# Kernel optimization log

Hardware: AMD Instinct MI355X
Metric: run time of the kernel (lower is better)

The kernel has to match this reference:

```python
import jax, jax.numpy as jnp
import numpy as np

# --- model dims (from init args) ---
LAYERS = 6
LEAF = 2 ** (LAYERS - 1)        # 32
M_LEN = 128
CAM_NUM = 2
MAIN_CAM = 0
LATENT = 48
H_LAT = 2048                    # LatentNet hidden
H_BR = 512                      # ChooseBranchNet hidden
B = 16384

# Path bits: for leaf i, bit at classifier depth d (root->leaf order) is
# (i >> (LAYERS-2-d)) & 1. This is exactly what the search_table + double
# advanced-indexing gather in the torch code computes (heap tree routing).
_BITS = ((np.arange(LEAF)[:, None] >> np.arange(LAYERS - 2, -1, -1)[None, :]) & 1)  # [LEAF, LAYERS-1]
BITS = jnp.asarray(_BITS, dtype=jnp.int32)


def setup_inputs() -> dict:
    key = jax.random.key(0)
    ks = jax.random.split(key, 9)
    s = lambda fan: 1.0 / np.sqrt(fan)
    return {
        "batch_data": jax.random.normal(ks[0], (B, CAM_NUM, M_LEN), dtype=jnp.float32),
        # LatentNet: [B, 2*M_LEN] -> hidden -> LEAF*LATENT
        "Wl1": jax.random.normal(ks[1], (2 * M_LEN, H_LAT), dtype=jnp.float32) * s(2 * M_LEN),
        "bl1": jnp.zeros((H_LAT,), dtype=jnp.float32),
        "Wl2": jax.random.normal(ks[2], (H_LAT, LEAF * LATENT), dtype=jnp.float32) * s(H_LAT),
        "bl2": jnp.zeros((LEAF * LATENT,), dtype=jnp.float32),
        # ChooseBranchNet (shared across the LAYERS-1 classifier slots): M_LEN -> hidden -> 2
        "Wb1": jax.random.normal(ks[3], (M_LEN, H_BR), dtype=jnp.float32) * s(M_LEN),
        "bb1": jnp.zeros((H_BR,), dtype=jnp.float32),
        "Wb2": jax.random.normal(ks[4], (H_BR, 2), dtype=jnp.float32) * s(H_BR),
        "bb2": jnp.zeros((2,), dtype=jnp.float32),
    }


def reference(batch_data, Wl1, bl1, Wl2, bl2, Wb1, bb1, Wb2, bb2):
    bsz = batch_data.shape[0]
    # expand_measurements: main cam repeated (LAYERS-1) times -> [B, LAYERS-1, M_LEN]
    main = batch_data[:, MAIN_CAM]                                  # [B, M_LEN]
    x_br = jnp.broadcast_to(main[:, None, :], (bsz, LAYERS - 1, M_LEN))
    # ChooseBranchNet -> per-layer 2-way probabilities
    h = jax.nn.relu(jnp.einsum('blm,mh->blh', x_br, Wb1) + bb1)
    p = jax.nn.softmax(jnp.einsum('blh,ho->blo', h, Wb2) + bb2, axis=-1)  # [B, L-1, 2]
    # Tree gates: product of path-branch probabilities along root->leaf path.
    comp = jnp.where(BITS[None] == 1, p[:, None, :, 1], p[:, None, :, 0])  # [B, LEAF, L-1]
    gates = jnp.prod(comp, axis=-1)                                        # [B, LEAF]
    # top-1 routing (argsort(...)[:, -1] as in the torch code)
    router = jnp.argsort(gates, axis=-1)[:, -1]                            # [B]
    # LatentNet on concatenated two-camera measurements
    x2 = jnp.concatenate([batch_data[:, 0], batch_data[:, 1]], axis=-1)    # [B, 2*M_LEN]
    hl = jax.nn.relu(x2 @ Wl1 + bl1)
    nn_latent = (hl @ Wl2 + bl2).reshape(bsz, LEAF, LATENT)
    # scatter-select per-sample leaf latent (replaces the torch.where loop)
    select = jnp.take_along_axis(nn_latent, router[:, None, None], axis=1)[:, 0]  # [B, LATENT]
    return select
```

## Files before the change

kernel.cpp:

```cpp
#include <hip/hip_runtime.h>
#include <stdint.h>

typedef short bf16x8 __attribute__((ext_vector_type(8)));
typedef float f32x4 __attribute__((ext_vector_type(4)));

#define NROWS 16384
#define K1DIM 256
#define N1DIM 2048
#define N2DIM 96
#define MARGIN 0.03f

#define GLD16(g, l) __builtin_amdgcn_global_load_lds( \
    (const __attribute__((address_space(1))) uint32_t*)(g), \
    (__attribute__((address_space(3))) uint32_t*)(l), 16, 0, 0)

__device__ __forceinline__ ushort f2bf(float x) {
  union { float f; uint32_t u; } c; c.f = x;
  uint32_t u = c.u;
  return (ushort)((u + 0x7FFFu + ((u >> 16) & 1u)) >> 16);
}

__global__ __launch_bounds__(256) void k0_convert(
    const float* __restrict__ bd, const float* __restrict__ Wl1,
    const float* __restrict__ Wl2, const float* __restrict__ Wb1,
    ushort* __restrict__ x2bf, ushort* __restrict__ wl1t,
    ushort* __restrict__ w2t, ushort* __restrict__ wb1t) {
  int i = blockIdx.x * 256 + threadIdx.x;
  if (i < NROWS * 256) x2bf[i] = f2bf(bd[i]);
  if (i < 2048 * 256) {
    int n = i >> 8, k = i & 255;
    wl1t[i] = f2bf(Wl1[k * 2048 + n]);
  }
  if (i < 96 * 2048) {
    int j = i >> 11, k = i & 2047;
    int col = (j < 48) ? j : (1440 + j);
    w2t[i] = f2bf(Wl2[k * 1536 + col]);
  }
  if (i < 512 * 128) {
    int j = i >> 7, m = i & 127;
    wb1t[i] = f2bf(Wb1[m * 512 + j]);
  }
}

__global__ __launch_bounds__(256) void k1a_score(
    const ushort* __restrict__ x2bf, const ushort* __restrict__ wb1t,
    const float* __restrict__ bb1, const float* __restrict__ Wb2,
    float* __restrict__ part) {
  __shared__ __align__(1024) ushort As[128 * 64];
  __shared__ __align__(1024) ushort Bs[128 * 64];
  const int t = threadIdx.x, ln = t & 63, wv = t >> 6;
  const int m0 = blockIdx.y << 7;
  const int n0 = blockIdx.x << 7;
  const int wm = (wv >> 1) << 6, wn = (wv & 1) << 6;
  const int rsub = ln >> 3, kc8 = ln & 7;
  const int q = ln >> 4, rr = ln & 15;

  f32x4 acc[4][4] = {};

  for (int k0 = 0; k0 < 128; k0 += 64) {
#pragma unroll
    for (int i = 0; i < 4; i++) {
      int inst = (wv << 2) + i;
      int row = (inst << 3) + rsub;
      GLD16(x2bf + (size_t)(m0 + row) * 256 + k0 + (kc8 << 3), As + (inst << 9));
      GLD16(wb1t + (size_t)(n0 + row) * 128 + k0 + (kc8 << 3), Bs + (inst << 9));
    }
    __syncthreads();
#pragma unroll
    for (int kk = 0; kk < 2; kk++) {
      int kb = ((kk << 2) + q) << 3;
      bf16x8 af[4], bfr[4];
#pragma unroll
      for (int mi = 0; mi < 4; mi++)
        af[mi] = *(const bf16x8*)(As + (((wm + (mi << 4) + rr)) << 6) + kb);
#pragma unroll
      for (int ni = 0; ni < 4; ni++)
        bfr[ni] = *(const bf16x8*)(Bs + (((wn + (ni << 4) + rr)) << 6) + kb);
#pragma unroll
      for (int mi = 0; mi < 4; mi++)
#pragma unroll
        for (int ni = 0; ni < 4; ni++)
          acc[mi][ni] = __builtin_amdgcn_mfma_f32_16x16x32_bf16(
              af[mi], bfr[ni], acc[mi][ni], 0, 0, 0);
    }
    __syncthreads();
  }

  float s4[4][4] = {};
#pragma unroll
  for (int ni = 0; ni < 4; ni++) {
    int col = n0 + wn + (ni << 4) + rr;
    float bias = bb1[col];
    float wdv = Wb2[col * 2 + 1] - Wb2[col * 2];
#pragma unroll
    for (int mi = 0; mi < 4; mi++) {
      f32x4 a = acc[mi][ni];
#pragma unroll
      for (int v = 0; v < 4; v++)
        s4[mi][v] += fmaxf(a[v] + bias, 0.f) * wdv;
    }
  }
#pragma unroll
  for (int off = 1; off <= 8; off <<= 1)
#pragma unroll
    for (int mi = 0; mi < 4; mi++)
#pragma unroll
      for (int v = 0; v < 4; v++)
        s4[mi][v] += __shfl_xor(s4[mi][v], off);

  if (rr == 0) {
    float* dst = part + (size_t)(blockIdx.x * 2 + (wv & 1)) * NROWS +
                 m0 + wm + (q << 2);
#pragma unroll
    for (int mi = 0; mi < 4; mi++) {
      float4 v4 = make_float4(s4[mi][0], s4[mi][1], s4[mi][2], s4[mi][3]);
      *(float4*)(dst + (mi << 4)) = v4;
    }
  }
}

__global__ __launch_bounds__(256) void k1b_classify(
    const float* __restrict__ part, const float* __restrict__ bb2,
    int* __restrict__ router, int* __restrict__ list, int* __restrict__ counter) {
  int t = blockIdx.x * 256 + threadIdx.x;
  float s = bb2[1] - bb2[0];
#pragma unroll
  for (int i = 0; i < 8; i++) s += part[i * NROWS + t];
  router[t] = (s >= 0.f) ? 1 : 0;
  if (fabsf(s) < MARGIN) {
    int idx = atomicAdd(counter, 1);
    list[idx] = t;
  }
}

__global__ __launch_bounds__(256) void k1c_recheck(
    const float* __restrict__ bd, const float* __restrict__ Wb1,
    const float* __restrict__ Wb2, const float* __restrict__ bb1,
    const float* __restrict__ bb2, const int* __restrict__ list,
    const int* __restrict__ counter, int* __restrict__ router) {
  const int ln = threadIdx.x & 63;
  const int wid = (blockIdx.x * 256 + threadIdx.x) >> 6;
  const int count = *counter;
  const float c = bb2[1] - bb2[0];

  for (int base = wid * 4; base < count; base += 512 * 4) {
    int rows[4];
#pragma unroll
    for (int r = 0; r < 4; r++) {
      int idx = base + r;
      rows[r] = list[(idx < count) ? idx : base];
    }
    float acc[4][8];
#pragma unroll
    for (int r = 0; r < 4; r++)
#pragma unroll
      for (int u = 0; u < 8; u++) acc[r][u] = 0.f;

    for (int m = 0; m < 128; m++) {
      float w[8];
#pragma unroll
      for (int u = 0; u < 8; u++) w[u] = Wb1[m * 512 + (u << 6) + ln];
#pragma unroll
      for (int r = 0; r < 4; r++) {
        float x = bd[(size_t)rows[r] * 256 + m];
#pragma unroll
        for (int u = 0; u < 8; u++) acc[r][u] = fmaf(x, w[u], acc[r][u]);
      }
    }
    float sc[4];
#pragma unroll
    for (int r = 0; r < 4; r++) {
      float s = 0.f;
#pragma unroll
      for (int u = 0; u < 8; u++) {
        int j = (u << 6) + ln;
        float wd = Wb2[j * 2 + 1] - Wb2[j * 2];
        s += fmaxf(acc[r][u] + bb1[j], 0.f) * wd;
      }
#pragma unroll
      for (int off = 1; off <= 32; off <<= 1) s += __shfl_xor(s, off);
      sc[r] = s + c;
    }
    if (ln == 0) {
#pragma unroll
      for (int r = 0; r < 4; r++)
        if (base + r < count) router[rows[r]] = (sc[r] >= 0.f) ? 1 : 0;
    }
  }
}

__global__ __launch_bounds__(256) void k2_fused(
    const ushort* __restrict__ x2bf, const ushort* __restrict__ wl1t,
    const ushort* __restrict__ w2t, const float* __restrict__ bl1,
    const float* __restrict__ bl2, const int* __restrict__ router,
    float* __restrict__ out) {
  __shared__ __align__(1024) ushort As[64 * 64];
  __shared__ __align__(1024) ushort Bs[128 * 64];
  __shared__ __align__(1024) ushort Ws[2 * 96 * 64];
  __shared__ __align__(1024) ushort Hs[64 * 128];
  const int t = threadIdx.x, ln = t & 63, wv = t >> 6;
  const int ks2 = blockIdx.x;
  const int m0 = blockIdx.y << 6;
  const int q = ln >> 4, rr = ln & 15;
  const int rsub = ln >> 3;
  const int swz8 = ((ln & 7) ^ rsub) << 3;

  f32x4 accP[6] = {};

  for (int nc = 0; nc < 8; nc++) {
    const int n0 = (ks2 << 10) + (nc << 7);

#pragma unroll
    for (int j = 0; j < 6; j++) {
      int inst = wv * 6 + j;
      int h = inst / 12;
      int r12 = inst - h * 12;
      GLD16(w2t + (size_t)((r12 << 3) + rsub) * 2048 + n0 + (h << 6) + swz8,
            Ws + h * 6144 + (r12 << 9));
    }

    f32x4 acc1[4][2] = {};
    for (int k0 = 0; k0 < K1DIM; k0 += 64) {
#pragma unroll
      for (int i = 0; i < 2; i++) {
        int inst = (wv << 1) + i;
        GLD16(x2bf + (size_t)(m0 + (inst << 3) + rsub) * K1DIM + k0 + swz8,
              As + (inst << 9));
      }
#pragma unroll
      for (int i = 0; i < 4; i++) {
        int inst = (wv << 2) + i;
        GLD16(wl1t + (size_t)(n0 + (inst << 3) + rsub) * K1DIM + k0 + swz8,
              Bs + (inst << 9));
      }
      __syncthreads();
#pragma unroll
      for (int kk = 0; kk < 2; kk++) {
        int slot = ((kk << 2) + q);
        bf16x8 af[4], bfr[2];
#pragma unroll
        for (int mi = 0; mi < 4; mi++)
          af[mi] = *(const bf16x8*)(As + (((mi << 4) + rr) << 6) +
                                    ((slot ^ (rr & 7)) << 3));
#pragma unroll
        for (int ni = 0; ni < 2; ni++)
          bfr[ni] = *(const bf16x8*)(Bs + (((wv << 5) + (ni << 4) + rr) << 6) +
                                     ((slot ^ (rr & 7)) << 3));
#pragma unroll
        for (int mi = 0; mi < 4; mi++)
#pragma unroll
          for (int ni = 0; ni < 2; ni++)
            acc1[mi][ni] = __builtin_amdgcn_mfma_f32_16x16x32_bf16(
                af[mi], bfr[ni], acc1[mi][ni], 0, 0, 0);
      }
      __syncthreads();
    }

#pragma unroll
    for (int ni = 0; ni < 2; ni++) {
      int lcol = (wv << 5) + (ni << 4) + rr;
      int slotc = lcol >> 3;
      float bias = bl1[n0 + lcol];
#pragma unroll
      for (int mi = 0; mi < 4; mi++) {
        f32x4 a = acc1[mi][ni];
#pragma unroll
        for (int v = 0; v < 4; v++) {
          int lrow = (mi << 4) + (q << 2) + v;
          Hs[(lrow << 7) + ((slotc ^ (lrow & 15)) << 3) + (rr & 7)] =
              f2bf(fmaxf(a[v] + bias, 0.f));
        }
      }
    }
    __syncthreads();

#pragma unroll
    for (int kk = 0; kk < 4; kk++) {
      int half = kk >> 1;
      int c2 = ((kk & 1) << 2) + q;
      int cH = (kk << 2) + q;
      bf16x8 ha = *(const bf16x8*)(Hs + (((wv << 4) + rr) << 7) +
                                   ((cH ^ rr) << 3));
#pragma unroll
      for (int ni = 0; ni < 6; ni++) {
        bf16x8 wb = *(const bf16x8*)(Ws + half * 6144 +
                                     (((ni << 4) + rr) << 6) +
                                     ((c2 ^ (rr & 7)) << 3));
        accP[ni] = __builtin_amdgcn_mfma_f32_16x16x32_bf16(ha, wb, accP[ni], 0, 0, 0);
      }
    }
    __syncthreads();
  }

  {
    int rowb = m0 + (wv << 4) + (q << 2);
#pragma unroll
    for (int v = 0; v < 4; v++) {
      int row = rowb + v;
      int sel = router[row];
      float v0 = sel ? accP[3][v] : accP[0][v];
      float v1 = sel ? accP[4][v] : accP[1][v];
      float v2 = sel ? accP[5][v] : accP[2][v];
      if (ks2 == 0) {
        int bb = sel ? 1488 : 0;
        v0 += bl2[bb + rr];
        v1 += bl2[bb + 16 + rr];
        v2 += bl2[bb + 32 + rr];
      }
      float* ob = out + (size_t)row * 48 + rr;
      atomicAdd(ob, v0);
      atomicAdd(ob + 16, v1);
      atomicAdd(ob + 32, v2);
    }
  }
}

extern "C" void kernel_launch(void* const* d_in, const int* in_sizes, int n_in,
                              void* d_out, int out_size, void* d_ws, size_t ws_size,
                              hipStream_t stream) {
  const float* bd  = (const float*)d_in[0];
  const float* Wl1 = (const float*)d_in[1];
  const float* bl1 = (const float*)d_in[2];
  const float* Wl2 = (const float*)d_in[3];
  const float* bl2 = (const float*)d_in[4];
  const float* Wb1 = (const float*)d_in[5];
  const float* bb1 = (const float*)d_in[6];
  const float* Wb2 = (const float*)d_in[7];
  const float* bb2 = (const float*)d_in[8];

  char* ws = (char*)d_ws;
  ushort* x2bf  = (ushort*)(ws);
  ushort* wl1t  = (ushort*)(ws + 8388608);
  ushort* w2t   = (ushort*)(ws + 9437184);
  int*    router= (int*)(ws + 89522176);
  ushort* wb1t  = (ushort*)(ws + 89587712);
  float*  part  = (float*)(ws + 89718784);
  int*    list  = (int*)(ws + 90243072);
  int*    counter=(int*)(ws + 90308608);
  float*  outp  = (float*)d_out;

  k0_convert<<<dim3(16384), dim3(256), 0, stream>>>(bd, Wl1, Wl2, Wb1,
                                                    x2bf, wl1t, w2t, wb1t);
  hipMemsetAsync(counter, 0, 4, stream);
  hipMemsetAsync(outp, 0, (size_t)out_size * 4, stream);
  k1a_score<<<dim3(4, 128), dim3(256), 0, stream>>>(x2bf, wb1t, bb1, Wb2, part);
  k1b_classify<<<dim3(64), dim3(256), 0, stream>>>(part, bb2, router, list, counter);
  k1c_recheck<<<dim3(128), dim3(256), 0, stream>>>(bd, Wb1, Wb2, bb1, bb2,
                                                   list, counter, router);
  k2_fused<<<dim3(2, 256), dim3(256), 0, stream>>>(x2bf, wl1t, w2t, bl1, bl2,
                                                   router, outp);
}
```

Measured before the change: 173.7 us.

## Enlarge fused MLP tile to 128 rows and split hidden dim four ways

Changes k2_fused from 64-row tiles with a two-way hidden split to 128-row tiles with a four-way hidden split. Each wave now computes a 64x64 sub-tile of the first GEMM, which gives more MFMA work per LDS fragment load, and the A/B staging buffers are aliased with the hidden-activation buffer to keep shared memory small. Launch bounds ask for two blocks per CU. The trade-off is twice as many atomicAdd partial sums into the output and more register pressure from the larger accumulators.

```diff
diff --git a/kernel.cpp b/kernel.cpp
--- a/kernel.cpp
+++ b/kernel.cpp
@@ -189,67 +189,65 @@
   }
 }
 
-__global__ __launch_bounds__(256) void k2_fused(
+__global__ __launch_bounds__(256, 2) void k2_fused(
     const ushort* __restrict__ x2bf, const ushort* __restrict__ wl1t,
     const ushort* __restrict__ w2t, const float* __restrict__ bl1,
     const float* __restrict__ bl2, const int* __restrict__ router,
     float* __restrict__ out) {
-  __shared__ __align__(1024) ushort As[64 * 64];
-  __shared__ __align__(1024) ushort Bs[128 * 64];
-  __shared__ __align__(1024) ushort Ws[2 * 96 * 64];
-  __shared__ __align__(1024) ushort Hs[64 * 128];
+  __shared__ __align__(1024) ushort U[16384];
+  __shared__ __align__(1024) ushort Wsm[12288];
+  ushort* As = U;
+  ushort* Bs = U + 8192;
+  ushort* Hs = U;
   const int t = threadIdx.x, ln = t & 63, wv = t >> 6;
   const int ks2 = blockIdx.x;
-  const int m0 = blockIdx.y << 6;
+  const int m0 = blockIdx.y << 7;
   const int q = ln >> 4, rr = ln & 15;
-  const int rsub = ln >> 3;
-  const int swz8 = ((ln & 7) ^ rsub) << 3;
-
-  f32x4 accP[6] = {};
-
-  for (int nc = 0; nc < 8; nc++) {
-    const int n0 = (ks2 << 10) + (nc << 7);
+  const int wm = (wv >> 1) << 6, wn = (wv & 1) << 6;
+  const int r8 = ln >> 3, s8 = ln & 7;
+  const int r16 = ln >> 4, s16 = ln & 15;
+
+  f32x4 accP[2][6] = {};
+
+  for (int nc = 0; nc < 4; nc++) {
+    const int n0 = (ks2 << 9) + (nc << 7);
 
 #pragma unroll
     for (int j = 0; j < 6; j++) {
       int inst = wv * 6 + j;
-      int h = inst / 12;
-      int r12 = inst - h * 12;
-      GLD16(w2t + (size_t)((r12 << 3) + rsub) * 2048 + n0 + (h << 6) + swz8,
-            Ws + h * 6144 + (r12 << 9));
-    }
-
-    f32x4 acc1[4][2] = {};
+      int r = (inst << 2) + r16;
+      GLD16(w2t + (size_t)r * 2048 + n0 + ((s16 ^ (r & 15)) << 3),
+            Wsm + (inst << 9));
+    }
+
+    f32x4 acc1[4][4] = {};
     for (int k0 = 0; k0 < K1DIM; k0 += 64) {
-#pragma unroll
-      for (int i = 0; i < 2; i++) {
-        int inst = (wv << 1) + i;
-        GLD16(x2bf + (size_t)(m0 + (inst << 3) + rsub) * K1DIM + k0 + swz8,
-              As + (inst << 9));
-      }
 #pragma unroll
       for (int i = 0; i < 4; i++) {
         int inst = (wv << 2) + i;
-        GLD16(wl1t + (size_t)(n0 + (inst << 3) + rsub) * K1DIM + k0 + swz8,
+        int r = (inst << 3) + r8;
+        GLD16(x2bf + (size_t)(m0 + r) * K1DIM + k0 + ((s8 ^ (r & 7)) << 3),
+              As + (inst << 9));
+        GLD16(wl1t + (size_t)(n0 + r) * K1DIM + k0 + ((s8 ^ (r & 7)) << 3),
               Bs + (inst << 9));
       }
       __syncthreads();
 #pragma unroll
       for (int kk = 0; kk < 2; kk++) {
-        int slot = ((kk << 2) + q);
-        bf16x8 af[4], bfr[2];
+        int c = (kk << 2) + q;
+        bf16x8 af[4], bfr[4];
 #pragma unroll
         for (int mi = 0; mi < 4; mi++)
-          af[mi] = *(const bf16x8*)(As + (((mi << 4) + rr) << 6) +
-                                    ((slot ^ (rr & 7)) << 3));
-#pragma unroll
-        for (int ni = 0; ni < 2; ni++)
-          bfr[ni] = *(const bf16x8*)(Bs + (((wv << 5) + (ni << 4) + rr) << 6) +
-                                     ((slot ^ (rr & 7)) << 3));
+          af[mi] = *(const bf16x8*)(As + ((wm + (mi << 4) + rr) << 6) +
+                                    ((c ^ (rr & 7)) << 3));
+#pragma unroll
+        for (int ni = 0; ni < 4; ni++)
+          bfr[ni] = *(const bf16x8*)(Bs + ((wn + (ni << 4) + rr) << 6) +
+                                     ((c ^ (rr & 7)) << 3));
 #pragma unroll
         for (int mi = 0; mi < 4; mi++)
 #pragma unroll
-          for (int ni = 0; ni < 2; ni++)
+          for (int ni = 0; ni < 4; ni++)
             acc1[mi][ni] = __builtin_amdgcn_mfma_f32_16x16x32_bf16(
                 af[mi], bfr[ni], acc1[mi][ni], 0, 0, 0);
       }
@@ -257,18 +255,17 @@
     }
 
 #pragma unroll
-    for (int ni = 0; ni < 2; ni++) {
-      int lcol = (wv << 5) + (ni << 4) + rr;
-      int slotc = lcol >> 3;
-      float bias = bl1[n0 + lcol];
+    for (int ni = 0; ni < 4; ni++) {
+      int col = wn + (ni << 4) + rr;
+      float bias = bl1[n0 + col];
 #pragma unroll
       for (int mi = 0; mi < 4; mi++) {
         f32x4 a = acc1[mi][ni];
 #pragma unroll
         for (int v = 0; v < 4; v++) {
-          int lrow = (mi << 4) + (q << 2) + v;
-          Hs[(lrow << 7) + ((slotc ^ (lrow & 15)) << 3) + (rr & 7)] =
-              f2bf(fmaxf(a[v] + bias, 0.f));
+          int row = wm + (mi << 4) + (q << 2) + v;
+          int s = (col >> 3) ^ (row & 15);
+          Hs[(row << 7) + (s << 3) + (col & 7)] = f2bf(fmaxf(a[v] + bias, 0.f));
         }
       }
     }
@@ -276,31 +273,36 @@
 
 #pragma unroll
     for (int kk = 0; kk < 4; kk++) {
-      int half = kk >> 1;
-      int c2 = ((kk & 1) << 2) + q;
-      int cH = (kk << 2) + q;
-      bf16x8 ha = *(const bf16x8*)(Hs + (((wv << 4) + rr) << 7) +
-                                   ((cH ^ rr) << 3));
+      int c = (kk << 2) + q;
+      bf16x8 ha[2];
+#pragma unroll
+      for (int g = 0; g < 2; g++) {
+        int row = (wv << 5) + (g << 4) + rr;
+        ha[g] = *(const bf16x8*)(Hs + (row << 7) + ((c ^ rr) << 3));
+      }
 #pragma unroll
       for (int ni = 0; ni < 6; ni++) {
-        bf16x8 wb = *(const bf16x8*)(Ws + half * 6144 +
-                                     (((ni << 4) + rr) << 6) +
-                                     ((c2 ^ (rr & 7)) << 3));
-        accP[ni] = __builtin_amdgcn_mfma_f32_16x16x32_bf16(ha, wb, accP[ni], 0, 0, 0);
+        int row = (ni << 4) + rr;
+        bf16x8 wb = *(const bf16x8*)(Wsm + (row << 7) + ((c ^ rr) << 3));
+#pragma unroll
+        for (int g = 0; g < 2; g++)
+          accP[g][ni] = __builtin_amdgcn_mfma_f32_16x16x32_bf16(
+              ha[g], wb, accP[g][ni], 0, 0, 0);
       }
     }
     __syncthreads();
   }
 
-  {
-    int rowb = m0 + (wv << 4) + (q << 2);
+#pragma unroll
+  for (int g = 0; g < 2; g++) {
+    int rowb = m0 + (wv << 5) + (g << 4) + (q << 2);
 #pragma unroll
     for (int v = 0; v < 4; v++) {
       int row = rowb + v;
       int sel = router[row];
-      float v0 = sel ? accP[3][v] : accP[0][v];
-      float v1 = sel ? accP[4][v] : accP[1][v];
-      float v2 = sel ? accP[5][v] : accP[2][v];
+      float v0 = sel ? accP[g][3][v] : accP[g][0][v];
+      float v1 = sel ? accP[g][4][v] : accP[g][1][v];
+      float v2 = sel ? accP[g][5][v] : accP[g][2][v];
       if (ks2 == 0) {
         int bb = sel ? 1488 : 0;
         v0 += bl2[bb + rr];
@@ -347,6 +349,6 @@
   k1b_classify<<<dim3(64), dim3(256), 0, stream>>>(part, bb2, router, list, counter);
   k1c_recheck<<<dim3(128), dim3(256), 0, stream>>>(bd, Wb1, Wb2, bb1, bb2,
                                                    list, counter, router);
-  k2_fused<<<dim3(2, 256), dim3(256), 0, stream>>>(x2bf, wl1t, w2t, bl1, bl2,
+  k2_fused<<<dim3(4, 128), dim3(256), 0, stream>>>(x2bf, wl1t, w2t, bl1, bl2,
                                                    router, outp);
 }
```

New measurement: 202.6 us. 1.17x slower.

## Widen k2 K-tile to 128, alias hidden tile onto B buffer, vectorize conversion

Applied to the files above, without the earlier changes.

The fused GEMM kernel now loads 128-wide K slices, so there are two K iterations per column chunk instead of four. This halves the barriers and load rounds. The second-layer weight tile is stored as 96 rows of 128 contiguous columns with a new XOR swizzle, and the hidden activation tile reuses the B-operand shared buffer. Launch bounds now request two blocks per CU to hold occupancy despite more LDS per block. Separately, the input conversion kernel converts four floats per thread using float4 loads and ushort4 stores, on a quarter of the blocks.

```diff
diff --git a/kernel.cpp b/kernel.cpp
--- a/kernel.cpp
+++ b/kernel.cpp
@@ -26,7 +26,12 @@
     ushort* __restrict__ x2bf, ushort* __restrict__ wl1t,
     ushort* __restrict__ w2t, ushort* __restrict__ wb1t) {
   int i = blockIdx.x * 256 + threadIdx.x;
-  if (i < NROWS * 256) x2bf[i] = f2bf(bd[i]);
+  {
+    float4 v = ((const float4*)bd)[i];
+    ushort4 o;
+    o.x = f2bf(v.x); o.y = f2bf(v.y); o.z = f2bf(v.z); o.w = f2bf(v.w);
+    ((ushort4*)x2bf)[i] = o;
+  }
   if (i < 2048 * 256) {
     int n = i >> 8, k = i & 255;
     wl1t[i] = f2bf(Wl1[k * 2048 + n]);
@@ -189,21 +194,21 @@
   }
 }
 
-__global__ __launch_bounds__(256) void k2_fused(
+__global__ __launch_bounds__(256, 2) void k2_fused(
     const ushort* __restrict__ x2bf, const ushort* __restrict__ wl1t,
     const ushort* __restrict__ w2t, const float* __restrict__ bl1,
     const float* __restrict__ bl2, const int* __restrict__ router,
     float* __restrict__ out) {
-  __shared__ __align__(1024) ushort As[64 * 64];
-  __shared__ __align__(1024) ushort Bs[128 * 64];
-  __shared__ __align__(1024) ushort Ws[2 * 96 * 64];
-  __shared__ __align__(1024) ushort Hs[64 * 128];
+  __shared__ __align__(1024) ushort Bsm[16384];
+  __shared__ __align__(1024) ushort Asm[8192];
+  __shared__ __align__(1024) ushort Wsm[12288];
+  ushort* Hs = Bsm;
   const int t = threadIdx.x, ln = t & 63, wv = t >> 6;
   const int ks2 = blockIdx.x;
   const int m0 = blockIdx.y << 6;
   const int q = ln >> 4, rr = ln & 15;
-  const int rsub = ln >> 3;
-  const int swz8 = ((ln & 7) ^ rsub) << 3;
+  const int sr4 = ln >> 4;
+  const int s16 = ln & 15;
 
   f32x4 accP[6] = {};
 
@@ -213,39 +218,43 @@
 #pragma unroll
     for (int j = 0; j < 6; j++) {
       int inst = wv * 6 + j;
-      int h = inst / 12;
-      int r12 = inst - h * 12;
-      GLD16(w2t + (size_t)((r12 << 3) + rsub) * 2048 + n0 + (h << 6) + swz8,
-            Ws + h * 6144 + (r12 << 9));
+      int r = (inst << 2) + sr4;
+      int c = s16 ^ (r & 7);
+      GLD16(w2t + (size_t)r * 2048 + n0 + (c << 3), Wsm + (inst << 9));
     }
 
     f32x4 acc1[4][2] = {};
-    for (int k0 = 0; k0 < K1DIM; k0 += 64) {
-#pragma unroll
-      for (int i = 0; i < 2; i++) {
-        int inst = (wv << 1) + i;
-        GLD16(x2bf + (size_t)(m0 + (inst << 3) + rsub) * K1DIM + k0 + swz8,
-              As + (inst << 9));
-      }
+#pragma unroll 1
+    for (int ks = 0; ks < 2; ks++) {
+      const int kg = ks << 7;
 #pragma unroll
       for (int i = 0; i < 4; i++) {
         int inst = (wv << 2) + i;
-        GLD16(wl1t + (size_t)(n0 + (inst << 3) + rsub) * K1DIM + k0 + swz8,
-              Bs + (inst << 9));
+        int r = (inst << 2) + sr4;
+        int c = s16 ^ (r & 7);
+        GLD16(x2bf + (size_t)(m0 + r) * K1DIM + kg + (c << 3),
+              Asm + (inst << 9));
+      }
+#pragma unroll
+      for (int i = 0; i < 8; i++) {
+        int inst = (wv << 3) + i;
+        int r = (inst << 2) + sr4;
+        int c = s16 ^ (r & 7);
+        GLD16(wl1t + (size_t)(n0 + r) * K1DIM + kg + (c << 3),
+              Bsm + (inst << 9));
       }
       __syncthreads();
 #pragma unroll
-      for (int kk = 0; kk < 2; kk++) {
-        int slot = ((kk << 2) + q);
+      for (int kk = 0; kk < 4; kk++) {
+        int c = (kk << 2) + q;
+        int sl = (c ^ (rr & 7)) << 3;
         bf16x8 af[4], bfr[2];
 #pragma unroll
         for (int mi = 0; mi < 4; mi++)
-          af[mi] = *(const bf16x8*)(As + (((mi << 4) + rr) << 6) +
-                                    ((slot ^ (rr & 7)) << 3));
+          af[mi] = *(const bf16x8*)(Asm + (((mi << 4) + rr) << 7) + sl);
 #pragma unroll
         for (int ni = 0; ni < 2; ni++)
-          bfr[ni] = *(const bf16x8*)(Bs + (((wv << 5) + (ni << 4) + rr) << 6) +
-                                     ((slot ^ (rr & 7)) << 3));
+          bfr[ni] = *(const bf16x8*)(Bsm + (((wv << 5) + (ni << 4) + rr) << 7) + sl);
 #pragma unroll
         for (int mi = 0; mi < 4; mi++)
 #pragma unroll
@@ -258,16 +267,15 @@
 
 #pragma unroll
     for (int ni = 0; ni < 2; ni++) {
-      int lcol = (wv << 5) + (ni << 4) + rr;
-      int slotc = lcol >> 3;
-      float bias = bl1[n0 + lcol];
+      int col = (wv << 5) + (ni << 4) + rr;
+      float bias = bl1[n0 + col];
 #pragma unroll
       for (int mi = 0; mi < 4; mi++) {
         f32x4 a = acc1[mi][ni];
 #pragma unroll
         for (int v = 0; v < 4; v++) {
-          int lrow = (mi << 4) + (q << 2) + v;
-          Hs[(lrow << 7) + ((slotc ^ (lrow & 15)) << 3) + (rr & 7)] =
+          int row = (mi << 4) + (q << 2) + v;
+          Hs[(row << 7) + (((col >> 3) ^ (row & 15)) << 3) + (col & 7)] =
               f2bf(fmaxf(a[v] + bias, 0.f));
         }
       }
@@ -276,16 +284,13 @@
 
 #pragma unroll
     for (int kk = 0; kk < 4; kk++) {
-      int half = kk >> 1;
-      int c2 = ((kk & 1) << 2) + q;
       int cH = (kk << 2) + q;
       bf16x8 ha = *(const bf16x8*)(Hs + (((wv << 4) + rr) << 7) +
                                    ((cH ^ rr) << 3));
 #pragma unroll
       for (int ni = 0; ni < 6; ni++) {
-        bf16x8 wb = *(const bf16x8*)(Ws + half * 6144 +
-                                     (((ni << 4) + rr) << 6) +
-                                     ((c2 ^ (rr & 7)) << 3));
+        bf16x8 wb = *(const bf16x8*)(Wsm + (((ni << 4) + rr) << 7) +
+                                     ((cH ^ (rr & 7)) << 3));
         accP[ni] = __builtin_amdgcn_mfma_f32_16x16x32_bf16(ha, wb, accP[ni], 0, 0, 0);
       }
     }
@@ -339,8 +344,8 @@
   int*    counter=(int*)(ws + 90308608);
   float*  outp  = (float*)d_out;
 
-  k0_convert<<<dim3(16384), dim3(256), 0, stream>>>(bd, Wl1, Wl2, Wb1,
-                                                    x2bf, wl1t, w2t, wb1t);
+  k0_convert<<<dim3(4096), dim3(256), 0, stream>>>(bd, Wl1, Wl2, Wb1,
+                                                   x2bf, wl1t, w2t, wb1t);
   hipMemsetAsync(counter, 0, 4, stream);
   hipMemsetAsync(outp, 0, (size_t)out_size * 4, stream);
   k1a_score<<<dim3(4, 128), dim3(256), 0, stream>>>(x2bf, wb1t, bb1, Wb2, part);
```

After: 170.8 us. No clear change (-1.7%).
